# Kernel optimization log

Hardware: AMD Instinct MI355X
Metric: run time of the kernel (lower is better)

The kernel has to match this reference:

```python
import jax, jax.numpy as jnp
import numpy as np

E, T, H, I = 8, 2048, 1024, 2048  # experts, tokens, hidden, intermediate


def setup_inputs() -> dict:
    key = jax.random.key(0)
    k1, k2, k3, k4, k5 = jax.random.split(key, 5)
    hiddens = jax.random.normal(k1, (T, H), dtype=jnp.float32)
    w1 = jax.random.normal(k2, (E, H, I), dtype=jnp.float32)  # gate proj
    w2 = jax.random.normal(k3, (E, I, H), dtype=jnp.float32)  # down proj
    w3 = jax.random.normal(k4, (E, H, I), dtype=jnp.float32)  # up proj
    # random partition of T tokens into E contiguous expert groups (sum == T)
    cuts = jnp.sort(jax.random.randint(k5, (E - 1,), 0, T + 1, dtype=jnp.int32))
    bounds = jnp.concatenate(
        [jnp.zeros((1,), jnp.int32), cuts, jnp.full((1,), T, jnp.int32)])
    batch_sizes = jnp.diff(bounds)  # [E], int32, sums to T
    return {"hiddens": hiddens, "w1_weight": w1, "w2_weight": w2,
            "w3_weight": w3, "batch_sizes": batch_sizes}


def reference(hiddens, w1_weight, w2_weight, w3_weight, batch_sizes):
    # grouped GEMM: tokens are contiguous per expert; group_sizes = batch_sizes
    up = jax.lax.ragged_dot(hiddens, w1_weight, batch_sizes)      # [T, I]
    up_r = jax.lax.ragged_dot(hiddens, w3_weight, batch_sizes)    # [T, I]
    gated = jax.nn.silu(up) * up_r                                # SiLU-gate fuse
    down = jax.lax.ragged_dot(gated, w2_weight, batch_sizes)      # [T, H]
    return down
```

## Files before the change

kernel.cpp:

```cpp
#include <hip/hip_runtime.h>
#include <hip/hip_bf16.h>
#include <stdint.h>


#define NE 8
#define NT 2048
#define NH 1024
#define NI 2048

typedef __attribute__((ext_vector_type(8))) short bh8;
typedef __attribute__((ext_vector_type(4))) short bh4;
typedef __attribute__((ext_vector_type(4))) float f32x4;
typedef __attribute__((ext_vector_type(4))) float float4v;

#define BARRIER() asm volatile("s_waitcnt lgkmcnt(0)\n\ts_barrier" ::: "memory")

static __device__ __forceinline__ unsigned short f2bf(float f) {
  __hip_bfloat16 h = __float2bfloat16(f);
  return *reinterpret_cast<unsigned short*>(&h);
}
static __device__ __forceinline__ float bf2f(unsigned short s) {
  return __uint_as_float(((unsigned int)s) << 16);
}

__global__ __launch_bounds__(256)
void cvt_h_kernel(const float* __restrict__ x, unsigned short* __restrict__ y) {
  int i = blockIdx.x * 256 + threadIdx.x;
  const float4v* xv = reinterpret_cast<const float4v*>(x);
  float4v a = xv[2 * i], b = xv[2 * i + 1];
  union { bh8 v; unsigned short u[8]; } o;
  o.u[0] = f2bf(a[0]); o.u[1] = f2bf(a[1]); o.u[2] = f2bf(a[2]); o.u[3] = f2bf(a[3]);
  o.u[4] = f2bf(b[0]); o.u[5] = f2bf(b[1]); o.u[6] = f2bf(b[2]); o.u[7] = f2bf(b[3]);
  reinterpret_cast<bh8*>(y)[i] = o.v;
}


template <int GATE>
__global__ __launch_bounds__(512, 2)
void moe_upg(const unsigned short* __restrict__ hb,
             const float* __restrict__ W,
             const int* __restrict__ bsz,
             const unsigned short* __restrict__ upin,
             unsigned short* __restrict__ O) {
  const int NWG = 4096;
  const int wg = (blockIdx.x & 7) * (NWG >> 3) + (blockIdx.x >> 3);
  const int mt = wg & 15;
  const int e = (wg >> 4) & 7;
  const int nt = wg >> 7;

  int off = 0;
#pragma unroll
  for (int j = 0; j < NE; ++j) { int v = bsz[j]; off += (j < e) ? v : 0; }
  const int te = bsz[e];
  if (mt * 128 >= te) return;

  const int tid = threadIdx.x;
  const int l = tid & 63, w = tid >> 6;
  const int wr = w >> 2, wc = w & 3;

  __shared__ __align__(16) unsigned short As[2][128 * 32];
  __shared__ __align__(16) unsigned short Bs[2][64 * 32];

  const int row0 = off + mt * 128;
  const int col0 = nt * 64;

  int gr = row0 + (tid >> 2); if (gr > NT - 1) gr = NT - 1;
  const unsigned short* agA = hb + (size_t)gr * NH + (tid & 3) * 8;
  const int awo = (tid >> 2) * 32 + (((tid & 3) ^ ((tid >> 3) & 3)) * 8);

  const float* wp = W + (size_t)e * NH * NI + (size_t)(4 * w) * NI + (col0 + l);
  const int bwo = l * 32 + (((w >> 1) ^ ((l >> 1) & 3)) * 8) + (w & 1) * 4;

  const int arow = wr * 64 + (l & 15);
  const int fslA = ((l >> 4) ^ ((l >> 1) & 3)) * 8;
  const int nbase = wc * 16 + (l & 15);
  const int bsl = ((l >> 4) ^ ((nbase >> 1) & 3)) * 8;

  f32x4 acc[4] = {};
  bh8 rA0, rA1;
  float rb0[4], rb1[4];

  auto issue = [&](int t, bh8& rA_, float (&rb_)[4]) {
    const int k0 = t * 32;
    rA_ = *(const bh8*)(agA + k0);
#pragma unroll
    for (int j = 0; j < 4; ++j) rb_[j] = *(wp + (size_t)(k0 + j) * NI);
  };
  auto stage = [&](int b, bh8& rA_, float (&rb_)[4]) {
    *(bh8*)(&As[b][awo]) = rA_;
    bh4 q;
#pragma unroll
    for (int j = 0; j < 4; ++j) q[j] = (short)f2bf(rb_[j]);
    *(bh4*)(&Bs[b][bwo]) = q;
  };
  auto mfma_step = [&](int b) {
    bh8 af[4];
#pragma unroll
    for (int m = 0; m < 4; ++m)
      af[m] = *(const bh8*)(&As[b][(arow + m * 16) * 32 + fslA]);
    bh8 bf = *(const bh8*)(&Bs[b][nbase * 32 + bsl]);
    __builtin_amdgcn_s_setprio(1);
#pragma unroll
    for (int m = 0; m < 4; ++m)
      acc[m] = __builtin_amdgcn_mfma_f32_16x16x32_bf16(af[m], bf, acc[m], 0, 0, 0);
    __builtin_amdgcn_s_setprio(0);
  };

  issue(0, rA0, rb0);
  issue(1, rA1, rb1);
  stage(0, rA0, rb0);
  BARRIER();

#pragma unroll 1
  for (int u = 0; u < 16; ++u) {
    const int t0 = 2 * u;
    if (t0 + 2 < 32) issue(t0 + 2, rA0, rb0);
    mfma_step(0);
    stage(1, rA1, rb1);
    BARRIER();
    if (t0 + 3 < 32) issue(t0 + 3, rA1, rb1);
    mfma_step(1);
    if (t0 + 2 < 32) stage(0, rA0, rb0);
    BARRIER();
  }

#pragma unroll
  for (int m = 0; m < 4; ++m) {
#pragma unroll
    for (int r = 0; r < 4; ++r) {
      int trow = mt * 128 + wr * 64 + m * 16 + (l >> 4) * 4 + r;
      if (trow < te) {
        size_t base = (size_t)(off + trow) * NI + col0 + wc * 16 + (l & 15);
        float g = acc[m][r];
        if (GATE) {
          float uu = bf2f(upin[base]);
          g = (uu / (1.f + __expf(-uu))) * g;
        }
        O[base] = f2bf(g);
      }
    }
  }
}

__global__ __launch_bounds__(512, 2)
void moe_down(const unsigned short* __restrict__ gated,
              const float* __restrict__ w2,
              const int* __restrict__ bsz,
              float* __restrict__ out) {
  const int NWG = 2048;
  const int wg = (blockIdx.x & 7) * (NWG >> 3) + (blockIdx.x >> 3);
  const int mt = wg & 15;
  const int e = (wg >> 4) & 7;
  const int nt = wg >> 7;

  int off = 0;
#pragma unroll
  for (int j = 0; j < NE; ++j) { int v = bsz[j]; off += (j < e) ? v : 0; }
  const int te = bsz[e];
  if (mt * 128 >= te) return;

  const int tid = threadIdx.x;
  const int l = tid & 63, w = tid >> 6;
  const int wr = w >> 2, wc = w & 3;

  __shared__ __align__(16) unsigned short As[2][128 * 32];
  __shared__ __align__(16) unsigned short Bs[2][64 * 32];

  const int row0 = off + mt * 128;
  const int col0 = nt * 64;

  int gr = row0 + (tid >> 2); if (gr > NT - 1) gr = NT - 1;
  const unsigned short* agA = gated + (size_t)gr * NI + (tid & 3) * 8;
  const int awo = (tid >> 2) * 32 + (((tid & 3) ^ ((tid >> 3) & 3)) * 8);

  const float* wp = w2 + (size_t)e * NI * NH + (size_t)(4 * w) * NH + (col0 + l);
  const int bwo = l * 32 + (((w >> 1) ^ ((l >> 1) & 3)) * 8) + (w & 1) * 4;

  const int arow = wr * 64 + (l & 15);
  const int fslA = ((l >> 4) ^ ((l >> 1) & 3)) * 8;
  const int nbase = wc * 16 + (l & 15);
  const int bsl = ((l >> 4) ^ ((nbase >> 1) & 3)) * 8;

  f32x4 acc[4] = {};
  bh8 rA0, rA1;
  float rb0[4], rb1[4];

  auto issue = [&](int t, bh8& rA_, float (&rb_)[4]) {
    const int k0 = t * 32;
    rA_ = *(const bh8*)(agA + k0);
#pragma unroll
    for (int j = 0; j < 4; ++j) rb_[j] = *(wp + (size_t)(k0 + j) * NH);
  };
  auto stage = [&](int b, bh8& rA_, float (&rb_)[4]) {
    *(bh8*)(&As[b][awo]) = rA_;
    bh4 q;
#pragma unroll
    for (int j = 0; j < 4; ++j) q[j] = (short)f2bf(rb_[j]);
    *(bh4*)(&Bs[b][bwo]) = q;
  };
  auto mfma_step = [&](int b) {
    bh8 af[4];
#pragma unroll
    for (int m = 0; m < 4; ++m)
      af[m] = *(const bh8*)(&As[b][(arow + m * 16) * 32 + fslA]);
    bh8 bf = *(const bh8*)(&Bs[b][nbase * 32 + bsl]);
    __builtin_amdgcn_s_setprio(1);
#pragma unroll
    for (int m = 0; m < 4; ++m)
      acc[m] = __builtin_amdgcn_mfma_f32_16x16x32_bf16(af[m], bf, acc[m], 0, 0, 0);
    __builtin_amdgcn_s_setprio(0);
  };

  issue(0, rA0, rb0);
  issue(1, rA1, rb1);
  stage(0, rA0, rb0);
  BARRIER();

#pragma unroll 1
  for (int u = 0; u < 32; ++u) {
    const int t0 = 2 * u;
    if (t0 + 2 < 64) issue(t0 + 2, rA0, rb0);
    mfma_step(0);
    stage(1, rA1, rb1);
    BARRIER();
    if (t0 + 3 < 64) issue(t0 + 3, rA1, rb1);
    mfma_step(1);
    if (t0 + 2 < 64) stage(0, rA0, rb0);
    BARRIER();
  }

#pragma unroll
  for (int m = 0; m < 4; ++m) {
#pragma unroll
    for (int r = 0; r < 4; ++r) {
      int trow = mt * 128 + wr * 64 + m * 16 + (l >> 4) * 4 + r;
      if (trow < te) {
        size_t base = (size_t)(off + trow) * NH + col0 + wc * 16 + (l & 15);
        out[base] = acc[m][r];
      }
    }
  }
}

extern "C" void kernel_launch(void* const* d_in, const int* in_sizes, int n_in,
                              void* d_out, int out_size, void* d_ws, size_t ws_size,
                              hipStream_t stream) {
  const float* hiddens = (const float*)d_in[0];
  const float* w1 = (const float*)d_in[1];
  const float* w2 = (const float*)d_in[2];
  const float* w3 = (const float*)d_in[3];
  const int* bsz = (const int*)d_in[4];
  float* out = (float*)d_out;

  unsigned short* hb = (unsigned short*)d_ws;
  unsigned short* up = hb + (size_t)NT * NH;
  unsigned short* gated = up + (size_t)NT * NI;

  cvt_h_kernel<<<dim3(NT * NH / 8 / 256), dim3(256), 0, stream>>>(hiddens, hb);
  moe_upg<0><<<dim3(4096), dim3(512), 0, stream>>>(hb, w1, bsz, up, up);
  moe_upg<1><<<dim3(4096), dim3(512), 0, stream>>>(hb, w3, bsz, up, gated);
  moe_down<<<dim3(2048), dim3(512), 0, stream>>>(gated, w2, bsz, out);
}
```

Measured before the change: 161.4 us.

## Use direct global-to-LDS loads with a four-stage pipeline in MoE GEMMs

Replaces the register-staged double buffer with __builtin_amdgcn_global_load_lds, which copies A (bf16) and the fp32 weight tile straight into shared memory. The loop becomes a four-buffer ring with three tiles in flight, governed by vmcnt waits and a single barrier per k-step. The fp32-to-bf16 weight conversion moves from the staging store to the LDS read inside the MFMA phase. This removes VGPR staging and the extra LDS write pass, at the cost of more LDS (fp32 B tiles, four stages), which may lower occupancy, plus extra scalar LDS reads and conversions per MFMA step.

```diff
diff --git a/kernel.cpp b/kernel.cpp
--- a/kernel.cpp
+++ b/kernel.cpp
@@ -9,11 +9,11 @@
 #define NI 2048
 
 typedef __attribute__((ext_vector_type(8))) short bh8;
-typedef __attribute__((ext_vector_type(4))) short bh4;
 typedef __attribute__((ext_vector_type(4))) float f32x4;
 typedef __attribute__((ext_vector_type(4))) float float4v;
 
-#define BARRIER() asm volatile("s_waitcnt lgkmcnt(0)\n\ts_barrier" ::: "memory")
+#define AS1 __attribute__((address_space(1)))
+#define AS3 __attribute__((address_space(3)))
 
 static __device__ __forceinline__ unsigned short f2bf(float f) {
   __hip_bfloat16 h = __float2bfloat16(f);
@@ -42,6 +42,7 @@
              const int* __restrict__ bsz,
              const unsigned short* __restrict__ upin,
              unsigned short* __restrict__ O) {
+  const int NP = 32;
   const int NWG = 4096;
   const int wg = (blockIdx.x & 7) * (NWG >> 3) + (blockIdx.x >> 3);
   const int mt = wg & 15;
@@ -58,70 +59,62 @@
   const int l = tid & 63, w = tid >> 6;
   const int wr = w >> 2, wc = w & 3;
 
-  __shared__ __align__(16) unsigned short As[2][128 * 32];
-  __shared__ __align__(16) unsigned short Bs[2][64 * 32];
+  __shared__ __align__(16) unsigned short As[4 * 128 * 32];
+  __shared__ __align__(16) float Bs[4 * 32 * 64];
 
   const int row0 = off + mt * 128;
   const int col0 = nt * 64;
 
   int gr = row0 + (tid >> 2); if (gr > NT - 1) gr = NT - 1;
-  const unsigned short* agA = hb + (size_t)gr * NH + (tid & 3) * 8;
-  const int awo = (tid >> 2) * 32 + (((tid & 3) ^ ((tid >> 3) & 3)) * 8);
-
-  const float* wp = W + (size_t)e * NH * NI + (size_t)(4 * w) * NI + (col0 + l);
-  const int bwo = l * 32 + (((w >> 1) ^ ((l >> 1) & 3)) * 8) + (w & 1) * 4;
+  const unsigned short* agA = hb + (size_t)gr * NH + (((tid & 3) ^ ((tid >> 3) & 3)) * 8);
+
+  const int kl = tid >> 4, nq = tid & 15;
+  const float* wpB = W + ((size_t)e * NH + kl) * NI + col0 + ((nq ^ ((kl >> 2) & 3)) << 2);
 
   const int arow = wr * 64 + (l & 15);
   const int fslA = ((l >> 4) ^ ((l >> 1) & 3)) * 8;
-  const int nbase = wc * 16 + (l & 15);
-  const int bsl = ((l >> 4) ^ ((nbase >> 1) & 3)) * 8;
+  const int cB = wc * 16 + (l & 15);
+  const int ksB = l >> 4;
 
   f32x4 acc[4] = {};
-  bh8 rA0, rA1;
-  float rb0[4], rb1[4];
-
-  auto issue = [&](int t, bh8& rA_, float (&rb_)[4]) {
+
+  auto issue = [&](int t, int b) {
     const int k0 = t * 32;
-    rA_ = *(const bh8*)(agA + k0);
-#pragma unroll
-    for (int j = 0; j < 4; ++j) rb_[j] = *(wp + (size_t)(k0 + j) * NI);
-  };
-  auto stage = [&](int b, bh8& rA_, float (&rb_)[4]) {
-    *(bh8*)(&As[b][awo]) = rA_;
-    bh4 q;
-#pragma unroll
-    for (int j = 0; j < 4; ++j) q[j] = (short)f2bf(rb_[j]);
-    *(bh4*)(&Bs[b][bwo]) = q;
-  };
-  auto mfma_step = [&](int b) {
+    __builtin_amdgcn_global_load_lds((const AS1 void*)(agA + k0),
+        (AS3 void*)(As + b * 4096 + w * 512), 16, 0, 0);
+    __builtin_amdgcn_global_load_lds((const AS1 void*)(wpB + (size_t)k0 * NI),
+        (AS3 void*)(Bs + b * 2048 + w * 256), 16, 0, 0);
+  };
+  auto mfma_phase = [&](int b) {
+    const unsigned short* Ab = As + b * 4096;
+    const float* Bb = Bs + b * 2048 + ksB * 512 + (cB & 3);
     bh8 af[4];
 #pragma unroll
     for (int m = 0; m < 4; ++m)
-      af[m] = *(const bh8*)(&As[b][(arow + m * 16) * 32 + fslA]);
-    bh8 bf = *(const bh8*)(&Bs[b][nbase * 32 + bsl]);
+      af[m] = *(const bh8*)(Ab + (arow + m * 16) * 32 + fslA);
+    union { bh8 v; unsigned short s[8]; } bfu;
+#pragma unroll
+    for (int j = 0; j < 8; ++j) {
+      const int g = (ksB * 2 + (j >> 2)) & 3;
+      bfu.s[j] = f2bf(Bb[j * 64 + (((cB >> 2) ^ g) << 2)]);
+    }
     __builtin_amdgcn_s_setprio(1);
 #pragma unroll
     for (int m = 0; m < 4; ++m)
-      acc[m] = __builtin_amdgcn_mfma_f32_16x16x32_bf16(af[m], bf, acc[m], 0, 0, 0);
+      acc[m] = __builtin_amdgcn_mfma_f32_16x16x32_bf16(af[m], bfu.v, acc[m], 0, 0, 0);
     __builtin_amdgcn_s_setprio(0);
   };
 
-  issue(0, rA0, rb0);
-  issue(1, rA1, rb1);
-  stage(0, rA0, rb0);
-  BARRIER();
-
+  issue(0, 0); issue(1, 1); issue(2, 2);
 #pragma unroll 1
-  for (int u = 0; u < 16; ++u) {
-    const int t0 = 2 * u;
-    if (t0 + 2 < 32) issue(t0 + 2, rA0, rb0);
-    mfma_step(0);
-    stage(1, rA1, rb1);
-    BARRIER();
-    if (t0 + 3 < 32) issue(t0 + 3, rA1, rb1);
-    mfma_step(1);
-    if (t0 + 2 < 32) stage(0, rA0, rb0);
-    BARRIER();
+  for (int p = 0; p < NP; ++p) {
+    if (p < NP - 2)       asm volatile("s_waitcnt vmcnt(4)" ::: "memory");
+    else if (p == NP - 2) asm volatile("s_waitcnt vmcnt(2)" ::: "memory");
+    else                  asm volatile("s_waitcnt vmcnt(0)" ::: "memory");
+    __builtin_amdgcn_sched_barrier(0);
+    __builtin_amdgcn_s_barrier();
+    if (p + 3 < NP) issue(p + 3, (p + 3) & 3);
+    mfma_phase(p & 3);
   }
 
 #pragma unroll
@@ -147,6 +140,7 @@
               const float* __restrict__ w2,
               const int* __restrict__ bsz,
               float* __restrict__ out) {
+  const int NP = 64;
   const int NWG = 2048;
   const int wg = (blockIdx.x & 7) * (NWG >> 3) + (blockIdx.x >> 3);
   const int mt = wg & 15;
@@ -163,70 +157,62 @@
   const int l = tid & 63, w = tid >> 6;
   const int wr = w >> 2, wc = w & 3;
 
-  __shared__ __align__(16) unsigned short As[2][128 * 32];
-  __shared__ __align__(16) unsigned short Bs[2][64 * 32];
+  __shared__ __align__(16) unsigned short As[4 * 128 * 32];
+  __shared__ __align__(16) float Bs[4 * 32 * 64];
 
   const int row0 = off + mt * 128;
   const int col0 = nt * 64;
 
   int gr = row0 + (tid >> 2); if (gr > NT - 1) gr = NT - 1;
-  const unsigned short* agA = gated + (size_t)gr * NI + (tid & 3) * 8;
-  const int awo = (tid >> 2) * 32 + (((tid & 3) ^ ((tid >> 3) & 3)) * 8);
-
-  const float* wp = w2 + (size_t)e * NI * NH + (size_t)(4 * w) * NH + (col0 + l);
-  const int bwo = l * 32 + (((w >> 1) ^ ((l >> 1) & 3)) * 8) + (w & 1) * 4;
+  const unsigned short* agA = gated + (size_t)gr * NI + (((tid & 3) ^ ((tid >> 3) & 3)) * 8);
+
+  const int kl = tid >> 4, nq = tid & 15;
+  const float* wpB = w2 + ((size_t)e * NI + kl) * NH + col0 + ((nq ^ ((kl >> 2) & 3)) << 2);
 
   const int arow = wr * 64 + (l & 15);
   const int fslA = ((l >> 4) ^ ((l >> 1) & 3)) * 8;
-  const int nbase = wc * 16 + (l & 15);
-  const int bsl = ((l >> 4) ^ ((nbase >> 1) & 3)) * 8;
+  const int cB = wc * 16 + (l & 15);
+  const int ksB = l >> 4;
 
   f32x4 acc[4] = {};
-  bh8 rA0, rA1;
-  float rb0[4], rb1[4];
-
-  auto issue = [&](int t, bh8& rA_, float (&rb_)[4]) {
+
+  auto issue = [&](int t, int b) {
     const int k0 = t * 32;
-    rA_ = *(const bh8*)(agA + k0);
-#pragma unroll
-    for (int j = 0; j < 4; ++j) rb_[j] = *(wp + (size_t)(k0 + j) * NH);
-  };
-  auto stage = [&](int b, bh8& rA_, float (&rb_)[4]) {
-    *(bh8*)(&As[b][awo]) = rA_;
-    bh4 q;
-#pragma unroll
-    for (int j = 0; j < 4; ++j) q[j] = (short)f2bf(rb_[j]);
-    *(bh4*)(&Bs[b][bwo]) = q;
-  };
-  auto mfma_step = [&](int b) {
+    __builtin_amdgcn_global_load_lds((const AS1 void*)(agA + k0),
+        (AS3 void*)(As + b * 4096 + w * 512), 16, 0, 0);
+    __builtin_amdgcn_global_load_lds((const AS1 void*)(wpB + (size_t)k0 * NH),
+        (AS3 void*)(Bs + b * 2048 + w * 256), 16, 0, 0);
+  };
+  auto mfma_phase = [&](int b) {
+    const unsigned short* Ab = As + b * 4096;
+    const float* Bb = Bs + b * 2048 + ksB * 512 + (cB & 3);
     bh8 af[4];
 #pragma unroll
     for (int m = 0; m < 4; ++m)
-      af[m] = *(const bh8*)(&As[b][(arow + m * 16) * 32 + fslA]);
-    bh8 bf = *(const bh8*)(&Bs[b][nbase * 32 + bsl]);
+      af[m] = *(const bh8*)(Ab + (arow + m * 16) * 32 + fslA);
+    union { bh8 v; unsigned short s[8]; } bfu;
+#pragma unroll
+    for (int j = 0; j < 8; ++j) {
+      const int g = (ksB * 2 + (j >> 2)) & 3;
+      bfu.s[j] = f2bf(Bb[j * 64 + (((cB >> 2) ^ g) << 2)]);
+    }
     __builtin_amdgcn_s_setprio(1);
 #pragma unroll
     for (int m = 0; m < 4; ++m)
-      acc[m] = __builtin_amdgcn_mfma_f32_16x16x32_bf16(af[m], bf, acc[m], 0, 0, 0);
+      acc[m] = __builtin_amdgcn_mfma_f32_16x16x32_bf16(af[m], bfu.v, acc[m], 0, 0, 0);
     __builtin_amdgcn_s_setprio(0);
   };
 
-  issue(0, rA0, rb0);
-  issue(1, rA1, rb1);
-  stage(0, rA0, rb0);
-  BARRIER();
-
+  issue(0, 0); issue(1, 1); issue(2, 2);
 #pragma unroll 1
-  for (int u = 0; u < 32; ++u) {
-    const int t0 = 2 * u;
-    if (t0 + 2 < 64) issue(t0 + 2, rA0, rb0);
-    mfma_step(0);
-    stage(1, rA1, rb1);
-    BARRIER();
-    if (t0 + 3 < 64) issue(t0 + 3, rA1, rb1);
-    mfma_step(1);
-    if (t0 + 2 < 64) stage(0, rA0, rb0);
-    BARRIER();
+  for (int p = 0; p < NP; ++p) {
+    if (p < NP - 2)       asm volatile("s_waitcnt vmcnt(4)" ::: "memory");
+    else if (p == NP - 2) asm volatile("s_waitcnt vmcnt(2)" ::: "memory");
+    else                  asm volatile("s_waitcnt vmcnt(0)" ::: "memory");
+    __builtin_amdgcn_sched_barrier(0);
+    __builtin_amdgcn_s_barrier();
+    if (p + 3 < NP) issue(p + 3, (p + 3) & 3);
+    mfma_phase(p & 3);
   }
 
 #pragma unroll
```

New measurement: 239.1 us. +48.2%, slower.
